# Optimization experiments

Measured on AMD Instinct MI355X. Metric: run time of the kernel, lower is better.

## Reference

```python
import jax, jax.numpy as jnp
import numpy as np

B, T, D, H = 2, 2048, 1024, 16
DH = D // H
SCALE = DH ** -0.5
NEG_INF = float(np.finfo(np.float32).min)


def setup_inputs() -> dict:
    key = jax.random.key(0)
    ks = jax.random.split(key, 8)
    query = jax.random.normal(ks[0], (B, T, D), dtype=jnp.float32)
    key_t = jax.random.normal(ks[1], (B, T, D), dtype=jnp.float32)
    value = jax.random.normal(ks[2], (B, T, D), dtype=jnp.float32)
    # causal mask: True means blocked (upper triangle)
    mask = ~jnp.tril(jnp.ones((T, T), dtype=bool))
    # key padding: pad tail beyond a random valid length per batch row
    lens = jax.random.randint(ks[3], (B,), T // 2, T)
    key_padding_mask = jnp.arange(T)[None, :] >= lens[:, None]  # [B, T] True = pad
    s = D ** -0.5
    Wq = jax.random.normal(ks[4], (D, D), dtype=jnp.float32) * s
    Wk = jax.random.normal(ks[5], (D, D), dtype=jnp.float32) * s
    Wv = jax.random.normal(ks[6], (D, D), dtype=jnp.float32) * s
    Wo = jax.random.normal(ks[7], (D, D), dtype=jnp.float32) * s
    return {"query": query, "key": key_t, "value": value, "mask": mask,
            "key_padding_mask": key_padding_mask, "Wq": Wq, "Wk": Wk, "Wv": Wv, "Wo": Wo}


def reference(query, key, value, mask, key_padding_mask, Wq, Wk, Wv, Wo):
    # Linear (no bias): y = x @ W.T, then split heads -> [B, H, T, DH]
    def proj(x, W, Tlen):
        return jnp.einsum('btd,ed->bte', x, W).reshape(B, Tlen, H, DH).transpose(0, 2, 1, 3)

    q = proj(query, Wq, T)
    k = proj(key, Wk, T)
    v = proj(value, Wv, T)

    attn = jnp.einsum('bhqd,bhkd->bhqk', q, k) * SCALE  # [B, H, Tq, Tk]
    attn = jnp.where(mask[None, None, :, :], -jnp.inf, attn)
    attn = jnp.where(key_padding_mask[:, None, None, :], -jnp.inf, attn)
    # rows of batches where ALL keys are padding: zero the logits (softmax -> uniform)
    all_masked = jnp.all(key_padding_mask, axis=-1)[:, None, None, None]
    attn = jnp.where(all_masked, 0.0, attn)

    p = jax.nn.softmax(attn, axis=-1)
    p = jnp.where(jnp.isnan(p), 0.0, p)  # scrub NaN rows (all -inf)

    out = jnp.einsum('bhqk,bhkd->bhqd', p, v)
    out = out.transpose(0, 2, 1, 3).reshape(B, T, D)
    return jnp.einsum('btd,ed->bte', out, Wo)
```

## Files before the change

### kernel.cpp

```cpp
#include <hip/hip_runtime.h>

#define B_  2
#define T_  2048
#define D_  1024
#define H_  16
#define DH_ 64
#define M_  4096

typedef _Float16 f16;
typedef _Float16 f16x8 __attribute__((ext_vector_type(8)));
typedef _Float16 f16x4 __attribute__((ext_vector_type(4)));
typedef float    f32x4  __attribute__((ext_vector_type(4)));
typedef float    f32x16 __attribute__((ext_vector_type(16)));
typedef unsigned int u32;

__device__ __forceinline__ void async_ld16(const void* g, void* l) {
  __builtin_amdgcn_global_load_lds(
      (const __attribute__((address_space(1))) unsigned int*)g,
      (__attribute__((address_space(3))) unsigned int*)l,
      16, 0, 0);
}

__device__ __forceinline__ u32 pkh(f16 a, f16 b) {
  union { f16 h[2]; u32 u; } x; x.h[0] = a; x.h[1] = b; return x.u;
}

__global__ __launch_bounds__(256) void convert_all(
    const float* __restrict__ q, const float* __restrict__ k, const float* __restrict__ v,
    const float* __restrict__ wq, const float* __restrict__ wk, const float* __restrict__ wv,
    const float* __restrict__ wo, const void* __restrict__ kpm_raw,
    f16* __restrict__ xh, f16* __restrict__ wh, int* __restrict__ lens_out) {
  int bid = blockIdx.x;
  if (bid >= 8192) {
    int b = bid - 8192;
    __shared__ int s_c8, s_c32;
    if (threadIdx.x == 0) { s_c8 = 0; s_c32 = 0; }
    __syncthreads();
    int tid = threadIdx.x, lane = tid & 63;
    {
      const unsigned char* k8 = (const unsigned char*)kpm_raw + (long)b * T_;
      int cnt = 0;
      for (int j = tid; j < T_; j += 256) cnt += (k8[j] == 0) ? 1 : 0;
#pragma unroll
      for (int off = 1; off < 64; off <<= 1) cnt += __shfl_xor(cnt, off);
      if (lane == 0) atomicAdd(&s_c8, cnt);
    }
    {
      const int* k32 = (const int*)kpm_raw + (long)b * T_;
      int cnt = 0;
      for (int j = tid; j < T_; j += 256) cnt += (k32[j] == 0) ? 1 : 0;
#pragma unroll
      for (int off = 1; off < 64; off <<= 1) cnt += __shfl_xor(cnt, off);
      if (lane == 0) atomicAdd(&s_c32, cnt);
    }
    __syncthreads();
    if (tid == 0) lens_out[b] = (s_c8 == T_) ? s_c32 : s_c8;
    return;
  }
  const float* src;
  f16* dst;
  long base;
  if (bid < 6144) {
    int r = bid >> 11;
    src = (r == 0) ? q : (r == 1) ? k : v;
    dst = xh + (long)r * 4194304;
    base = (long)(bid & 2047) * 2048;
  } else {
    int r = (bid - 6144) >> 9;
    src = (r == 0) ? wq : (r == 1) ? wk : (r == 2) ? wv : wo;
    dst = wh + (long)r * 1048576;
    base = (long)((bid - 6144) & 511) * 2048;
  }
  long e = base + (long)threadIdx.x * 8;
  const float4* s4 = (const float4*)(src + e);
  float4 f0 = s4[0], f1 = s4[1];
  f16x8 o;
  o[0] = (f16)f0.x; o[1] = (f16)f0.y; o[2] = (f16)f0.z; o[3] = (f16)f0.w;
  o[4] = (f16)f1.x; o[5] = (f16)f1.y; o[6] = (f16)f1.z; o[7] = (f16)f1.w;
  *(f16x8*)(dst + e) = o;
}

__global__ __launch_bounds__(256) void gemm_k(
    const f16* __restrict__ Abase, const f16* __restrict__ Wbase,
    f16* __restrict__ Qb, f16* __restrict__ Kb, f16* __restrict__ Vt,
    float* __restrict__ Co, int which) {
  __shared__ __align__(16) f16 As[2][128][32];
  __shared__ __align__(16) f16 Bs[2][128][32];
  const int K = 1024, N = 1024;

  int gx = gridDim.x, gy = gridDim.y;
  int nwg = gx * gy * gridDim.z;
  int bid = blockIdx.x + gx * (blockIdx.y + gy * blockIdx.z);
  int cpx = nwg >> 3;
  int wg = (bid & 7) * cpx + (bid >> 3);
  int bz = wg / (gx * gy);
  int rem = wg - bz * gx * gy;
  int by = rem / gx, bx = rem - by * gx;

  int mode;
  const f16 *A, *W;
  if (which) { mode = 3; A = Abase; W = Wbase; }
  else {
    mode = bz;
    A = Abase + (long)bz * 4194304;
    W = Wbase + (long)bz * 1048576;
  }
  int m0 = by * 128, n0 = bx * 128;
  int tid = threadIdx.x, lane = tid & 63, w = tid >> 6;
  int wm = w >> 1, wn = w & 1;

  int srow = w * 16 + (lane >> 2);
  int scol = (lane & 3) * 8;
  const f16* pa = A + (long)(m0 + srow) * K + scol;
  const f16* pb = W + (long)(n0 + srow) * K + scol;

  f32x4 acc[4][4] = {};
  int row = lane & 15, kq = (lane >> 4) * 8;

  auto STAGE = [&](int k0, int bsel) {
    async_ld16(pa + k0,          &As[bsel][srow][scol]);
    async_ld16(pa + 64 * K + k0, &As[bsel][64 + srow][scol]);
    async_ld16(pb + k0,          &Bs[bsel][srow][scol]);
    async_ld16(pb + 64 * K + k0, &Bs[bsel][64 + srow][scol]);
  };

  STAGE(0, 0);
  asm volatile("s_waitcnt vmcnt(0)" ::: "memory");
  __builtin_amdgcn_s_barrier();

  int cur = 0;
  for (int k0 = 0; k0 < K; k0 += 32) {
    if (k0 + 32 < K) STAGE(k0 + 32, cur ^ 1);
    f16x8 af[4], bfr[4];
#pragma unroll
    for (int m = 0; m < 4; m++) af[m] = *(const f16x8*)&As[cur][wm * 64 + m * 16 + row][kq];
#pragma unroll
    for (int n = 0; n < 4; n++) bfr[n] = *(const f16x8*)&Bs[cur][wn * 64 + n * 16 + row][kq];
#pragma unroll
    for (int m = 0; m < 4; m++)
#pragma unroll
      for (int n = 0; n < 4; n++)
        acc[m][n] = __builtin_amdgcn_mfma_f32_16x16x32_f16(af[m], bfr[n], acc[m][n], 0, 0, 0);
    asm volatile("s_waitcnt vmcnt(0)" ::: "memory");
    __builtin_amdgcn_s_barrier();
    cur ^= 1;
  }

  int r0 = (lane >> 4) * 4;
#pragma unroll
  for (int m = 0; m < 4; m++) {
    int gmb = m0 + wm * 64 + m * 16 + r0;
#pragma unroll
    for (int n = 0; n < 4; n++) {
      int gn = n0 + wn * 64 + n * 16 + row;
      if (mode == 0) {
#pragma unroll
        for (int i = 0; i < 4; i++)
          Qb[(long)(gmb + i) * N + gn] = (f16)(acc[m][n][i] * 0.125f);
      } else if (mode == 1) {
#pragma unroll
        for (int i = 0; i < 4; i++)
          Kb[(long)(gmb + i) * N + gn] = (f16)acc[m][n][i];
      } else if (mode == 2) {
        int b = gmb >> 11;
        int t = gmb & 2047;
        int h = gn >> 6, dh = gn & 63;
        f16x4 pk;
#pragma unroll
        for (int i = 0; i < 4; i++) pk[i] = (f16)acc[m][n][i];
        *(f16x4*)&Vt[(long)((b * 16 + h) * 64 + dh) * 2048 + t] = pk;
      } else {
#pragma unroll
        for (int i = 0; i < 4; i++)
          Co[(long)(gmb + i) * N + gn] = acc[m][n][i];
      }
    }
  }
}

__global__ __launch_bounds__(256) void attn_k(
    const f16* __restrict__ Q, const f16* __restrict__ Kp,
    const f16* __restrict__ Vt, const int* __restrict__ Lens,
    f16* __restrict__ Ao) {
  __shared__ __align__(16) f16 Kl[2][4096];
  __shared__ __align__(16) f16 Vl[2][4096];

  int tid = threadIdx.x, lane = tid & 63, w = tid >> 6;
  int qm = (gridDim.x - 1) - blockIdx.x;
  int bh = blockIdx.y;
  int b = bh >> 4, h = bh & 15;
  int r31 = lane & 31, hi = lane >> 5, hi8 = hi * 8;

  int len = Lens[b];
  int q0 = qm * 128;
  int q0w = q0 + w * 32;
  int gq = q0w + r31;

  int blk_kmax = min(q0 + 128, len);
  int wav_kmax = min(q0w + 32, len);
  int NT = (blk_kmax + 63) >> 6;

  const f16* Qh = Q  + (long)b * T_ * D_ + h * 64;
  const f16* Kh = Kp + (long)b * T_ * D_ + h * 64;
  const f16* Vh = Vt + (long)(b * 16 + h) * 64 * T_;

  int srow = w * 16 + (lane >> 3);
  int sc8  = ((lane & 7) ^ ((lane >> 3) & 7)) * 8;
  int ldst = w * 1024 + lane * 8;

  int coff[4];
#pragma unroll
  for (int t = 0; t < 4; t++) coff[t] = ((2 * t + hi) ^ (r31 & 7)) * 8;

  auto STAGE = [&](int t, int bsel) {
    int kb = t * 64;
#pragma unroll
    for (int s = 0; s < 2; s++) {
      int row = srow + s * 8;
      async_ld16(Kh + (long)(kb + row) * D_ + sc8, &Kl[bsel][ldst + s * 512]);
      async_ld16(Vh + (long)row * T_ + kb + sc8,   &Vl[bsel][ldst + s * 512]);
    }
  };

  STAGE(0, 0);
  f16x8 qf[4];
#pragma unroll
  for (int t = 0; t < 4; t++)
    qf[t] = *(const f16x8*)(Qh + (long)gq * D_ + t * 16 + hi8);

  f32x16 o0 = {}, o1 = {};
  float mrun = -1e30f, lrun = 0.f;

  asm volatile("s_waitcnt vmcnt(0)" ::: "memory");
  __syncthreads();

  for (int t = 0; t < NT; t++) {
    int cur = t & 1;
    if (t + 1 < NT) STAGE(t + 1, cur ^ 1);

    int kb = t * 64;
    if (kb < wav_kmax) {
      f32x16 s0 = {}, s1 = {};
#pragma unroll
      for (int tq = 0; tq < 4; tq++) {
        f16x8 k0 = *(const f16x8*)&Kl[cur][(r31)      * 64 + coff[tq]];
        f16x8 k1 = *(const f16x8*)&Kl[cur][(32 + r31) * 64 + coff[tq]];
        s0 = __builtin_amdgcn_mfma_f32_32x32x16_f16(k0, qf[tq], s0, 0, 0, 0);
        s1 = __builtin_amdgcn_mfma_f32_32x32x16_f16(k1, qf[tq], s1, 0, 0, 0);
      }

      bool needmask = (kb + 64 > q0w) || (kb + 64 > len);
      float sv[32];
      if (needmask) {
#pragma unroll
        for (int r = 0; r < 16; r++) {
          int pat = (r & 3) + 8 * (r >> 2) + 4 * hi;
          int gk0 = kb + pat, gk1 = kb + 32 + pat;
          sv[r]      = (gk0 > gq || gk0 >= len) ? -1e30f : s0[r];
          sv[16 + r] = (gk1 > gq || gk1 >= len) ? -1e30f : s1[r];
        }
      } else {
#pragma unroll
        for (int r = 0; r < 16; r++) { sv[r] = s0[r]; sv[16 + r] = s1[r]; }
      }

      float mx = fmaxf(sv[0], sv[1]);
#pragma unroll
      for (int r = 2; r < 32; r++) mx = fmaxf(mx, sv[r]);
      mx = fmaxf(mx, __shfl_xor(mx, 32));

      float mnew = fmaxf(mrun, mx);
      float sf = __expf(mrun - mnew);
      mrun = mnew;

      f16 p16[32];
      float ps[4] = {0.f, 0.f, 0.f, 0.f};
#pragma unroll
      for (int r = 0; r < 32; r++) {
        float p = __expf(sv[r] - mnew);
        f16 hp = (f16)p;
        p16[r] = hp;
        ps[r & 3] += (float)hp;
      }
      float psum = (ps[0] + ps[1]) + (ps[2] + ps[3]);
      lrun = lrun * sf + psum + __shfl_xor(psum, 32);

      o0 *= sf;
      o1 *= sf;

      u32 A0 = pkh(p16[0],  p16[1]),  A1 = pkh(p16[2],  p16[3]);
      u32 B0 = pkh(p16[4],  p16[5]),  B1 = pkh(p16[6],  p16[7]);
      u32 C0 = pkh(p16[8],  p16[9]),  C1 = pkh(p16[10], p16[11]);
      u32 D0 = pkh(p16[12], p16[13]), D1 = pkh(p16[14], p16[15]);
      u32 E0 = pkh(p16[16], p16[17]), E1 = pkh(p16[18], p16[19]);
      u32 F0 = pkh(p16[20], p16[21]), F1 = pkh(p16[22], p16[23]);
      u32 G0 = pkh(p16[24], p16[25]), G1 = pkh(p16[26], p16[27]);
      u32 H0 = pkh(p16[28], p16[29]), H1 = pkh(p16[30], p16[31]);
      u32 sA0 = __shfl_xor(A0, 32), sA1 = __shfl_xor(A1, 32);
      u32 sB0 = __shfl_xor(B0, 32), sB1 = __shfl_xor(B1, 32);
      u32 sC0 = __shfl_xor(C0, 32), sC1 = __shfl_xor(C1, 32);
      u32 sD0 = __shfl_xor(D0, 32), sD1 = __shfl_xor(D1, 32);
      u32 sE0 = __shfl_xor(E0, 32), sE1 = __shfl_xor(E1, 32);
      u32 sF0 = __shfl_xor(F0, 32), sF1 = __shfl_xor(F1, 32);
      u32 sG0 = __shfl_xor(G0, 32), sG1 = __shfl_xor(G1, 32);
      u32 sH0 = __shfl_xor(H0, 32), sH1 = __shfl_xor(H1, 32);

      union { u32 w[4]; f16x8 v; } f00, f01, f10, f11;
      f00.w[0] = hi ? sB0 : A0;  f00.w[1] = hi ? sB1 : A1;
      f00.w[2] = hi ? B0 : sA0;  f00.w[3] = hi ? B1 : sA1;
      f01.w[0] = hi ? sD0 : C0;  f01.w[1] = hi ? sD1 : C1;
      f01.w[2] = hi ? D0 : sC0;  f01.w[3] = hi ? D1 : sC1;
      f10.w[0] = hi ? sF0 : E0;  f10.w[1] = hi ? sF1 : E1;
      f10.w[2] = hi ? F0 : sE0;  f10.w[3] = hi ? F1 : sE1;
      f11.w[0] = hi ? sH0 : G0;  f11.w[1] = hi ? sH1 : G1;
      f11.w[2] = hi ? H0 : sG0;  f11.w[3] = hi ? H1 : sG1;

      f16x8 v00 = *(const f16x8*)&Vl[cur][(r31)      * 64 + coff[0]];
      f16x8 v01 = *(const f16x8*)&Vl[cur][(r31)      * 64 + coff[1]];
      f16x8 v02 = *(const f16x8*)&Vl[cur][(r31)      * 64 + coff[2]];
      f16x8 v03 = *(const f16x8*)&Vl[cur][(r31)      * 64 + coff[3]];
      f16x8 v10 = *(const f16x8*)&Vl[cur][(32 + r31) * 64 + coff[0]];
      f16x8 v11 = *(const f16x8*)&Vl[cur][(32 + r31) * 64 + coff[1]];
      f16x8 v12 = *(const f16x8*)&Vl[cur][(32 + r31) * 64 + coff[2]];
      f16x8 v13 = *(const f16x8*)&Vl[cur][(32 + r31) * 64 + coff[3]];

      o0 = __builtin_amdgcn_mfma_f32_32x32x16_f16(v00, f00.v, o0, 0, 0, 0);
      o0 = __builtin_amdgcn_mfma_f32_32x32x16_f16(v01, f01.v, o0, 0, 0, 0);
      o0 = __builtin_amdgcn_mfma_f32_32x32x16_f16(v02, f10.v, o0, 0, 0, 0);
      o0 = __builtin_amdgcn_mfma_f32_32x32x16_f16(v03, f11.v, o0, 0, 0, 0);
      o1 = __builtin_amdgcn_mfma_f32_32x32x16_f16(v10, f00.v, o1, 0, 0, 0);
      o1 = __builtin_amdgcn_mfma_f32_32x32x16_f16(v11, f01.v, o1, 0, 0, 0);
      o1 = __builtin_amdgcn_mfma_f32_32x32x16_f16(v12, f10.v, o1, 0, 0, 0);
      o1 = __builtin_amdgcn_mfma_f32_32x32x16_f16(v13, f11.v, o1, 0, 0, 0);
    }

    asm volatile("s_waitcnt vmcnt(0)" ::: "memory");
    __syncthreads();
  }

  float linv = 1.f / lrun;
  f16* Aob = Ao + (long)(b * T_ + gq) * D_ + h * 64 + 4 * hi;
#pragma unroll
  for (int g = 0; g < 4; g++) {
    f16x4 s0, s1;
#pragma unroll
    for (int i = 0; i < 4; i++) {
      s0[i] = (f16)(o0[g * 4 + i] * linv);
      s1[i] = (f16)(o1[g * 4 + i] * linv);
    }
    *(f16x4*)(Aob + 8 * g)      = s0;
    *(f16x4*)(Aob + 32 + 8 * g) = s1;
  }
}

extern "C" void kernel_launch(void* const* d_in, const int* in_sizes, int n_in,
                              void* d_out, int out_size, void* d_ws, size_t ws_size,
                              hipStream_t stream) {
  const float* q  = (const float*)d_in[0];
  const float* k  = (const float*)d_in[1];
  const float* v  = (const float*)d_in[2];
  const void* kpm = d_in[4];
  const float* wq = (const float*)d_in[5];
  const float* wk = (const float*)d_in[6];
  const float* wv = (const float*)d_in[7];
  const float* wo = (const float*)d_in[8];

  char* ws = (char*)d_ws;
  f16* Xh = (f16*)(ws);
  f16* Wh = (f16*)(ws + 25165824);
  f16* Qb = (f16*)(ws + 33554432);
  f16* Kb = (f16*)(ws + 41943040);
  f16* Vt = (f16*)(ws + 50331648);
  f16* Ao = (f16*)(ws + 58720256);
  int* Lens = (int*)d_out;

  convert_all<<<8194, 256, 0, stream>>>(q, k, v, wq, wk, wv, wo, kpm, Xh, Wh, Lens);

  gemm_k<<<dim3(8, 32, 3), 256, 0, stream>>>(Xh, Wh, Qb, Kb, Vt, nullptr, 0);

  attn_k<<<dim3(T_ / 128, B_ * H_), 256, 0, stream>>>(Qb, Kb, Vt, Lens, Ao);

  gemm_k<<<dim3(8, 32, 1), 256, 0, stream>>>(Ao, Wh + 3 * 1048576, nullptr, nullptr,
                                             nullptr, (float*)d_out, 1);
}
```

Before: 139.6 us.

## Fold log2e into Q scale, use exp2 and packed RTZ conversion, reorder attention grid

Q is pre-scaled by SCALE*log2(e) so the softmax can use exp2 in place of exp. This drops a multiply per element. Probabilities stay in fp32 for the row sum and are packed to f16 pairs with a single cvt_pkrtz, which replaces separate per-element conversions. The row max becomes a tree reduction for more ILP, and the attention grid is reordered so heads vary fastest and query tiles run heavy-then-light for better load balance. Round-toward-zero packing and summing unrounded probabilities change numerics slightly.

```diff
diff --git a/kernel.cpp b/kernel.cpp
--- a/kernel.cpp
+++ b/kernel.cpp
@@ -10,6 +10,7 @@
 typedef _Float16 f16;
 typedef _Float16 f16x8 __attribute__((ext_vector_type(8)));
 typedef _Float16 f16x4 __attribute__((ext_vector_type(4)));
+typedef __fp16   fp16x2 __attribute__((ext_vector_type(2)));
 typedef float    f32x4  __attribute__((ext_vector_type(4)));
 typedef float    f32x16 __attribute__((ext_vector_type(16)));
 typedef unsigned int u32;
@@ -21,8 +22,10 @@
       16, 0, 0);
 }
 
-__device__ __forceinline__ u32 pkh(f16 a, f16 b) {
-  union { f16 h[2]; u32 u; } x; x.h[0] = a; x.h[1] = b; return x.u;
+__device__ __forceinline__ u32 pkrtz(float a, float b) {
+  union { fp16x2 h; u32 u; } x;
+  x.h = __builtin_amdgcn_cvt_pkrtz(a, b);
+  return x.u;
 }
 
 __global__ __launch_bounds__(256) void convert_all(
@@ -156,7 +159,7 @@
       if (mode == 0) {
 #pragma unroll
         for (int i = 0; i < 4; i++)
-          Qb[(long)(gmb + i) * N + gn] = (f16)(acc[m][n][i] * 0.125f);
+          Qb[(long)(gmb + i) * N + gn] = (f16)(acc[m][n][i] * 0.18033688f);
       } else if (mode == 1) {
 #pragma unroll
         for (int i = 0; i < 4; i++)
@@ -186,8 +189,9 @@
   __shared__ __align__(16) f16 Vl[2][4096];
 
   int tid = threadIdx.x, lane = tid & 63, w = tid >> 6;
-  int qm = (gridDim.x - 1) - blockIdx.x;
-  int bh = blockIdx.y;
+  int bh = blockIdx.x;
+  int j  = blockIdx.y;
+  int qm = (j < 8) ? (15 - j) : (j - 8);
   int b = bh >> 4, h = bh & 15;
   int r31 = lane & 31, hi = lane >> 5, hi8 = hi * 8;
 
@@ -264,23 +268,25 @@
         for (int r = 0; r < 16; r++) { sv[r] = s0[r]; sv[16 + r] = s1[r]; }
       }
 
-      float mx = fmaxf(sv[0], sv[1]);
-#pragma unroll
-      for (int r = 2; r < 32; r++) mx = fmaxf(mx, sv[r]);
-      mx = fmaxf(mx, __shfl_xor(mx, 32));
+      float t16[16];
+#pragma unroll
+      for (int r = 0; r < 16; r++) t16[r] = fmaxf(sv[r], sv[16 + r]);
+#pragma unroll
+      for (int s = 8; s > 0; s >>= 1)
+#pragma unroll
+        for (int r = 0; r < s; r++) t16[r] = fmaxf(t16[r], t16[r + s]);
+      float mx = fmaxf(t16[0], __shfl_xor(t16[0], 32));
 
       float mnew = fmaxf(mrun, mx);
-      float sf = __expf(mrun - mnew);
+      float sf = exp2f(mrun - mnew);
       mrun = mnew;
 
-      f16 p16[32];
+      float p[32];
       float ps[4] = {0.f, 0.f, 0.f, 0.f};
 #pragma unroll
       for (int r = 0; r < 32; r++) {
-        float p = __expf(sv[r] - mnew);
-        f16 hp = (f16)p;
-        p16[r] = hp;
-        ps[r & 3] += (float)hp;
+        p[r] = exp2f(sv[r] - mnew);
+        ps[r & 3] += p[r];
       }
       float psum = (ps[0] + ps[1]) + (ps[2] + ps[3]);
       lrun = lrun * sf + psum + __shfl_xor(psum, 32);
@@ -288,14 +294,14 @@
       o0 *= sf;
       o1 *= sf;
 
-      u32 A0 = pkh(p16[0],  p16[1]),  A1 = pkh(p16[2],  p16[3]);
-      u32 B0 = pkh(p16[4],  p16[5]),  B1 = pkh(p16[6],  p16[7]);
-      u32 C0 = pkh(p16[8],  p16[9]),  C1 = pkh(p16[10], p16[11]);
-      u32 D0 = pkh(p16[12], p16[13]), D1 = pkh(p16[14], p16[15]);
-      u32 E0 = pkh(p16[16], p16[17]), E1 = pkh(p16[18], p16[19]);
-      u32 F0 = pkh(p16[20], p16[21]), F1 = pkh(p16[22], p16[23]);
-      u32 G0 = pkh(p16[24], p16[25]), G1 = pkh(p16[26], p16[27]);
-      u32 H0 = pkh(p16[28], p16[29]), H1 = pkh(p16[30], p16[31]);
+      u32 A0 = pkrtz(p[0],  p[1]),  A1 = pkrtz(p[2],  p[3]);
+      u32 B0 = pkrtz(p[4],  p[5]),  B1 = pkrtz(p[6],  p[7]);
+      u32 C0 = pkrtz(p[8],  p[9]),  C1 = pkrtz(p[10], p[11]);
+      u32 D0 = pkrtz(p[12], p[13]), D1 = pkrtz(p[14], p[15]);
+      u32 E0 = pkrtz(p[16], p[17]), E1 = pkrtz(p[18], p[19]);
+      u32 F0 = pkrtz(p[20], p[21]), F1 = pkrtz(p[22], p[23]);
+      u32 G0 = pkrtz(p[24], p[25]), G1 = pkrtz(p[26], p[27]);
+      u32 H0 = pkrtz(p[28], p[29]), H1 = pkrtz(p[30], p[31]);
       u32 sA0 = __shfl_xor(A0, 32), sA1 = __shfl_xor(A1, 32);
       u32 sB0 = __shfl_xor(B0, 32), sB1 = __shfl_xor(B1, 32);
       u32 sC0 = __shfl_xor(C0, 32), sC1 = __shfl_xor(C1, 32);
@@ -378,7 +384,7 @@
 
   gemm_k<<<dim3(8, 32, 3), 256, 0, stream>>>(Xh, Wh, Qb, Kb, Vt, nullptr, 0);
 
-  attn_k<<<dim3(T_ / 128, B_ * H_), 256, 0, stream>>>(Qb, Kb, Vt, Lens, Ao);
+  attn_k<<<dim3(B_ * H_, T_ / 128), 256, 0, stream>>>(Qb, Kb, Vt, Lens, Ao);
 
   gemm_k<<<dim3(8, 32, 1), 256, 0, stream>>>(Ao, Wh + 3 * 1048576, nullptr, nullptr,
                                              nullptr, (float*)d_out, 1);
```

Result: no change. 140.5 us (median of 2 runs) (+0.6%).
